# Kernel tuning notes

Hardware: AMD Instinct MI355X
Metric: run time of the kernel (lower is better)

## Reference

```python
import jax, jax.numpy as jnp
import numpy as np

N_HEAD, D_MODEL, D_K, D_V = 16, 1024, 64, 64
BN_EPS = 1e-5
NEG_INF = -1e9


def setup_inputs() -> dict:
    key = jax.random.key(0)
    ks = jax.random.split(key, 10)
    B, L = 4, 1024
    q = jax.random.normal(ks[0], (B, L, D_MODEL), dtype=jnp.float32)
    k = jax.random.normal(ks[1], (B, L, D_MODEL), dtype=jnp.float32)
    v = jax.random.normal(ks[2], (B, L, D_MODEL), dtype=jnp.float32)
    attn_mask = jax.random.randint(ks[3], (B, L, L), 0, 2) == 1  # True -> masked out
    s = 1.0 / np.sqrt(D_MODEL)
    w_qs = jax.random.normal(ks[4], (N_HEAD, D_MODEL, D_K), dtype=jnp.float32) * s
    w_ks = jax.random.normal(ks[5], (N_HEAD, D_MODEL, D_K), dtype=jnp.float32) * s
    w_vs = jax.random.normal(ks[6], (N_HEAD, D_MODEL, D_V), dtype=jnp.float32) * s
    proj_w = jax.random.normal(ks[7], (D_MODEL, N_HEAD * D_V), dtype=jnp.float32) * s
    proj_b = jnp.zeros((D_MODEL,), dtype=jnp.float32)
    bn_gamma = jnp.ones((D_MODEL,), dtype=jnp.float32)
    bn_beta = jnp.zeros((D_MODEL,), dtype=jnp.float32)
    return {"q": q, "k": k, "v": v, "attn_mask": attn_mask,
            "w_qs": w_qs, "w_ks": w_ks, "w_vs": w_vs,
            "proj_w": proj_w, "proj_b": proj_b,
            "bn_gamma": bn_gamma, "bn_beta": bn_beta}


def reference(q, k, v, attn_mask, w_qs, w_ks, w_vs, proj_w, proj_b, bn_gamma, bn_beta):
    B, Lq, D = q.shape
    temper = jnp.asarray(np.sqrt(D), dtype=q.dtype)
    residual = q
    # per-head projections: (H, B, L, dk)
    qh = jnp.einsum('bld,hdk->hblk', q, w_qs)
    kh = jnp.einsum('bld,hdk->hblk', k, w_ks)
    vh = jnp.einsum('bld,hdv->hblv', v, w_vs)
    # scaled dot-product attention, temper = sqrt(d_model)
    scores = jnp.einsum('hbqk,hbsk->hbqs', qh, kh) / temper
    scores = jnp.where(attn_mask[None], NEG_INF, scores)
    attns = jax.nn.softmax(scores, axis=-1)  # (H, B, Lq, Lk)
    out_h = jnp.einsum('hbqs,hbsv->hbqv', attns, vh)  # (H, B, Lq, dv)
    # concat heads along feature dim in head order
    out = jnp.transpose(out_h, (1, 2, 0, 3)).reshape(B, Lq, N_HEAD * D_V)
    out = out @ proj_w.T + proj_b
    # residual + BatchNorm1d over channel dim (batch stats, training-mode math)
    x = out + residual  # (B, L, D)
    mean = jnp.mean(x, axis=(0, 1))
    var = jnp.var(x, axis=(0, 1))
    x = (x - mean) * jax.lax.rsqrt(var + BN_EPS) * bn_gamma + bn_beta
    attns_flat = attns.reshape(N_HEAD * B, Lq, -1)
    return x, attns_flat
```

## Files before the change

kernel.cpp:

```cpp
#include <hip/hip_runtime.h>

typedef unsigned short ushort;
typedef __attribute__((ext_vector_type(4))) float floatx4;
typedef __bf16 bf16x8 __attribute__((ext_vector_type(8)));
typedef __bf16 bf16x4 __attribute__((ext_vector_type(4)));
typedef float f32x4 __attribute__((ext_vector_type(4)));

constexpr int NB = 4;
constexpr int NL = 1024;
constexpr int ND = 1024;
constexpr int NH = 16;
constexpr int NDK = 64;

union B4 { bf16x4 v; unsigned long long ll; };

__device__ __forceinline__ void st_bf(ushort* dst, float f){
  union { __bf16 h; ushort u; } z; z.h = (__bf16)f; *dst = z.u;
}

#define MFMA(a,b,c) __builtin_amdgcn_mfma_f32_16x16x32_bf16((a),(b),(c),0,0,0)

__global__ __launch_bounds__(256) void k_prep(const float* __restrict__ q,
                                              const float* __restrict__ k,
                                              const float* __restrict__ v,
                                              const float* __restrict__ pw,
                                              const float* __restrict__ w0,
                                              const float* __restrict__ w1,
                                              const float* __restrict__ w2,
                                              const int* __restrict__ M,
                                              ushort* __restrict__ qb,
                                              ushort* __restrict__ kb,
                                              ushort* __restrict__ vb,
                                              ushort* __restrict__ pwb,
                                              ushort* __restrict__ t0,
                                              ushort* __restrict__ t1,
                                              ushort* __restrict__ t2,
                                              unsigned long long* __restrict__ MB,
                                              float* __restrict__ part){
  __shared__ ushort T[64][65];
  const int bid = blockIdx.x;
  const int tid = threadIdx.x;

  if (bid < 6656){
    const int a = (bid < 2048) ? 0 : (bid < 4096) ? 1 : (bid < 6144) ? 2 : 3;
    const int rel = bid - a * 2048;
    const float* src = (a == 0) ? q : (a == 1) ? k : (a == 2) ? v : pw;
    ushort* dst = (a == 0) ? qb : (a == 1) ? kb : (a == 2) ? vb : pwb;
    const size_t base = ((size_t)rel * 256 + tid) * 8;
    floatx4 v0 = *(const floatx4*)(src + base);
    floatx4 v1 = *(const floatx4*)(src + base + 4);
    bf16x8 o;
    #pragma unroll
    for (int j = 0; j < 4; j++){ o[j] = (__bf16)v0[j]; o[4 + j] = (__bf16)v1[j]; }
    *(bf16x8*)(dst + base) = o;
    return;
  }
  if (bid < 7424){
    const int r = bid - 6656;
    const int z = r >> 8;
    const int h = (r >> 4) & 15, k0 = (r & 15) * 64;
    const float* src = (z == 0) ? w0 : (z == 1) ? w1 : w2;
    ushort* dst = (z == 0) ? t0 : (z == 1) ? t1 : t2;
    const int qd = tid >> 6, lo = tid & 63;
    #pragma unroll
    for (int i = 0; i < 16; i++){
      int kl = qd + i * 4;
      float f = src[((size_t)h * 1024 + k0 + kl) * 64 + lo];
      union { __bf16 h2; ushort u; } zz; zz.h2 = (__bf16)f;
      T[kl][lo] = zz.u;
    }
    __syncthreads();
    #pragma unroll
    for (int i = 0; i < 16; i++){
      int dk = qd + i * 4;
      dst[((size_t)h * 64 + dk) * 1024 + k0 + lo] = T[lo][dk];
    }
    return;
  }
  if (bid < 11520){
    const int r = bid - 7424;
    #pragma unroll
    for (int rep = 0; rep < 4; rep++){
      const int gid = r * 1024 + rep * 256 + tid;
      const int widx = gid >> 6;
      int m = M[(size_t)widx * 64 + (gid & 63)];
      unsigned long long bal = __ballot(m != 0);
      if ((gid & 63) == 0) MB[widx] = bal;
    }
    return;
  }
  *(floatx4*)(part + tid * 8) = f32x4{0.f, 0.f, 0.f, 0.f};
  *(floatx4*)(part + tid * 8 + 4) = f32x4{0.f, 0.f, 0.f, 0.f};
}

__global__ __launch_bounds__(256) void k_projm(const ushort* __restrict__ qbp,
                                               const ushort* __restrict__ kbp,
                                               const ushort* __restrict__ vbp,
                                               const ushort* __restrict__ wqT,
                                               const ushort* __restrict__ wkT,
                                               const ushort* __restrict__ wvT,
                                               ushort* __restrict__ qh,
                                               ushort* __restrict__ kh,
                                               ushort* __restrict__ vt){
  __shared__ bf16x8 Ach[8 * 128];
  __shared__ bf16x8 Bch[8 * 128];
  const int z = blockIdx.z;
  const ushort* Xb = (z == 0) ? qbp : (z == 1) ? kbp : vbp;
  const ushort* WT = (z == 0) ? wqT : (z == 1) ? wkT : wvT;
  const int tid = threadIdx.x;
  const int lane = tid & 63, wid = tid >> 6;
  const int g = lane >> 4, c = lane & 15;
  const int d = blockIdx.y * 8 + blockIdx.x;
  const int tile = (d & 7) * 32 + (d >> 3);
  const int row0 = (tile >> 3) * 128, col0 = (tile & 7) * 128;
  const int wm = (wid >> 1) * 64, wn = (wid & 1) * 64;

  f32x4 zero = {0.f, 0.f, 0.f, 0.f};
  f32x4 acc[4][4];
  #pragma unroll
  for (int i = 0; i < 4; i++)
    #pragma unroll
    for (int j = 0; j < 4; j++) acc[i][j] = zero;

  for (int k0 = 0; k0 < ND; k0 += 64){
    #pragma unroll
    for (int i = 0; i < 4; i++){
      int e = tid + i * 256;
      int kc = e & 7, m = e >> 3;
      Ach[kc * 128 + (m ^ kc)] = *(const bf16x8*)(Xb + (size_t)(row0 + m) * ND + k0 + kc * 8);
    }
    #pragma unroll
    for (int i = 0; i < 4; i++){
      int e = tid + i * 256;
      int kc = e & 7, n = e >> 3;
      int hh = (col0 + n) >> 6, dk = (col0 + n) & 63;
      Bch[kc * 128 + (n ^ kc)] = *(const bf16x8*)(WT + ((size_t)(hh << 6) + dk) * 1024 + k0 + kc * 8);
    }
    __syncthreads();
    bf16x8 bfr[4][2];
    #pragma unroll
    for (int ni = 0; ni < 4; ni++){
      int n = wn + ni * 16 + c;
      bfr[ni][0] = Bch[g * 128 + (n ^ g)];
      bfr[ni][1] = Bch[(4 + g) * 128 + (n ^ (4 + g))];
    }
    #pragma unroll
    for (int mi = 0; mi < 4; mi++){
      int m = wm + mi * 16 + c;
      bf16x8 a0 = Ach[g * 128 + (m ^ g)];
      bf16x8 a1 = Ach[(4 + g) * 128 + (m ^ (4 + g))];
      #pragma unroll
      for (int ni = 0; ni < 4; ni++){
        acc[mi][ni] = MFMA(a0, bfr[ni][0], acc[mi][ni]);
        acc[mi][ni] = MFMA(a1, bfr[ni][1], acc[mi][ni]);
      }
    }
    __syncthreads();
  }
  if (z == 2){
    #pragma unroll
    for (int mi = 0; mi < 4; mi++){
      #pragma unroll
      for (int ni = 0; ni < 4; ni++){
        int n = col0 + wn + ni * 16 + c;
        int hh = n >> 6, dk = n & 63;
        int m0 = row0 + wm + mi * 16 + g * 4;
        int bb = m0 >> 10, l = m0 & 1023;
        B4 o;
        #pragma unroll
        for (int r = 0; r < 4; r++) o.v[r] = (__bf16)acc[mi][ni][r];
        *(unsigned long long*)(vt + (((size_t)hh * NB + bb) * 64 + dk) * 1024 + l) = o.ll;
      }
    }
  } else {
    ushort* OUT = (z == 0) ? qh : kh;
    #pragma unroll
    for (int mi = 0; mi < 4; mi++){
      #pragma unroll
      for (int ni = 0; ni < 4; ni++){
        #pragma unroll
        for (int r = 0; r < 4; r++){
          int m = row0 + wm + mi * 16 + g * 4 + r;
          int n = col0 + wn + ni * 16 + c;
          int bb = m >> 10, ls = m & 1023;
          int hh = n >> 6, dk = n & 63;
          st_bf(OUT + (((size_t)hh * NB + bb) * NL + ls) * NDK + dk, acc[mi][ni][r]);
        }
      }
    }
  }
}

__global__ __launch_bounds__(256, 4) void k_attn(const ushort* __restrict__ QH,
                                                 const ushort* __restrict__ KH,
                                                 const ushort* __restrict__ VT,
                                                 const unsigned* __restrict__ MB,
                                                 float* __restrict__ ATT,
                                                 ushort* __restrict__ CTX){
  __shared__ bf16x8 Kch[512];
  __shared__ bf16x8 Vch[512];
  __shared__ ushort Ps[4][16][72];
  __shared__ unsigned Ms[64 * 33];
  const int tid = threadIdx.x;
  const int lane = tid & 63, wid = tid >> 6;
  const int g = lane >> 4, c = lane & 15;
  const int d = blockIdx.y * 16 + blockIdx.x;
  const int tile = (d & 7) * 128 + (d >> 3);
  const int hb = tile >> 4;
  const int q0 = (tile & 15) * 64;
  const int h = hb >> 2, b = hb & 3;

  const int q = q0 + wid * 16 + c;
  const size_t qkbase = (size_t)hb * NL;

  bf16x8 qf0 = *(const bf16x8*)(QH + (qkbase + q) * NDK + g * 8);
  bf16x8 qf1 = *(const bf16x8*)(QH + (qkbase + q) * NDK + 32 + g * 8);

  {
    const unsigned* mbase = MB + ((size_t)(b << 10) + q0) * 32;
    #pragma unroll
    for (int i = 0; i < 8; i++){
      int idx = tid + i * 256;
      int ql2 = idx >> 5, word = idx & 31;
      Ms[ql2 * 33 + word] = mbase[ql2 * 32 + word];
    }
  }
  const int ql = wid * 16 + c;
  const int mg = g * 4;

  float rs = 0.f;
  for (int t = 0; t < 16; ++t){
    __syncthreads();
    const ushort* ksrc = KH + (qkbase + t * 64) * NDK;
    #pragma unroll
    for (int i = 0; i < 2; i++){
      int idx = tid * 2 + i;
      int sr = idx >> 3, kc = idx & 7;
      Kch[sr * 8 + (kc ^ (sr & 7))] = *(const bf16x8*)(ksrc + idx * 8);
    }
    __syncthreads();
    #pragma unroll
    for (int sub2 = 0; sub2 < 4; ++sub2){
      int s = sub2 * 16 + c;
      bf16x8 kf0 = Kch[s * 8 + (g ^ (s & 7))];
      bf16x8 kf1 = Kch[s * 8 + ((4 + g) ^ (s & 7))];
      f32x4 a = {0.f, 0.f, 0.f, 0.f};
      a = MFMA(kf0, qf0, a);
      a = MFMA(kf1, qf1, a);
      unsigned w = Ms[ql * 33 + t * 2 + (sub2 >> 1)];
      unsigned bits4 = (w >> (((sub2 & 1) << 4) + mg)) & 0xFu;
      #pragma unroll
      for (int r = 0; r < 4; r++)
        rs += ((bits4 >> r) & 1u) ? 0.f : __expf(a[r] * (1.f / 32.f));
    }
  }
  rs += __shfl_xor(rs, 16);
  rs += __shfl_xor(rs, 32);
  const float invd = 1.f / rs;

  f32x4 zero = {0.f, 0.f, 0.f, 0.f};
  f32x4 acc[4];
  #pragma unroll
  for (int i = 0; i < 4; i++) acc[i] = zero;

  for (int t = 0; t < 16; ++t){
    __syncthreads();
    const ushort* ksrc = KH + (qkbase + t * 64) * NDK;
    #pragma unroll
    for (int i = 0; i < 2; i++){
      int idx = tid * 2 + i;
      int sr = idx >> 3, kc = idx & 7;
      Kch[sr * 8 + (kc ^ (sr & 7))] = *(const bf16x8*)(ksrc + idx * 8);
    }
    #pragma unroll
    for (int i = 0; i < 2; i++){
      int idx = tid + i * 256;
      int dv = idx >> 3, kc = idx & 7;
      Vch[kc * 64 + (dv ^ kc)] = *(const bf16x8*)(VT + ((size_t)hb * 64 + dv) * 1024 + t * 64 + kc * 8);
    }
    __syncthreads();
    #pragma unroll
    for (int sub2 = 0; sub2 < 4; ++sub2){
      int s = sub2 * 16 + c;
      bf16x8 kf0 = Kch[s * 8 + (g ^ (s & 7))];
      bf16x8 kf1 = Kch[s * 8 + ((4 + g) ^ (s & 7))];
      f32x4 a = {0.f, 0.f, 0.f, 0.f};
      a = MFMA(kf0, qf0, a);
      a = MFMA(kf1, qf1, a);
      unsigned w = Ms[ql * 33 + t * 2 + (sub2 >> 1)];
      unsigned bits4 = (w >> (((sub2 & 1) << 4) + mg)) & 0xFu;
      floatx4 pn;
      B4 pw;
      #pragma unroll
      for (int r = 0; r < 4; r++){
        float p = ((bits4 >> r) & 1u) ? 0.f : __expf(a[r] * (1.f / 32.f)) * invd;
        pn[r] = p;
        pw.v[r] = (__bf16)p;
      }
      __builtin_nontemporal_store(pn,
        (floatx4*)(ATT + ((size_t)hb * NL + q) * NL + (t * 4 + sub2) * 16 + g * 4));
      *(unsigned long long*)&Ps[wid][c][sub2 * 16 + g * 4] = pw.ll;
    }
    #pragma unroll
    for (int ss = 0; ss < 2; ++ss){
      bf16x8 afr = *(bf16x8*)&Ps[wid][c][ss * 32 + g * 8];
      #pragma unroll
      for (int ni = 0; ni < 4; ni++){
        int kcr = ss * 4 + g;
        bf16x8 vfr = Vch[kcr * 64 + ((ni * 16 + c) ^ kcr)];
        acc[ni] = MFMA(afr, vfr, acc[ni]);
      }
    }
  }

  #pragma unroll
  for (int ni = 0; ni < 4; ni++)
    #pragma unroll
    for (int r = 0; r < 4; r++){
      int qq = q0 + wid * 16 + g * 4 + r;
      int dv = ni * 16 + c;
      st_bf(CTX + ((size_t)b * NL + qq) * ND + h * NDK + dv, acc[ni][r]);
    }
}

__global__ __launch_bounds__(256) void k_projo(const ushort* __restrict__ CTX,
                                               const ushort* __restrict__ PWb,
                                               const float* __restrict__ PB,
                                               const float* __restrict__ RES,
                                               float* __restrict__ X,
                                               float* __restrict__ part){
  __shared__ bf16x8 Ach[8 * 128];
  __shared__ bf16x8 Bch[8 * 128];
  const int tid = threadIdx.x;
  const int lane = tid & 63, wid = tid >> 6;
  const int g = lane >> 4, c = lane & 15;
  const int d = blockIdx.y * 8 + blockIdx.x;
  const int tile = (d & 7) * 32 + (d >> 3);
  const int row0 = (tile >> 3) * 128, col0 = (tile & 7) * 128;
  const int wm = (wid >> 1) * 64, wn = (wid & 1) * 64;

  f32x4 zero = {0.f, 0.f, 0.f, 0.f};
  f32x4 acc[4][4];
  #pragma unroll
  for (int i = 0; i < 4; i++)
    #pragma unroll
    for (int j = 0; j < 4; j++) acc[i][j] = zero;

  for (int k0 = 0; k0 < ND; k0 += 64){
    #pragma unroll
    for (int i = 0; i < 4; i++){
      int e = tid + i * 256;
      int kc = e & 7, m = e >> 3;
      Ach[kc * 128 + (m ^ kc)] = *(const bf16x8*)(CTX + (size_t)(row0 + m) * ND + k0 + kc * 8);
    }
    #pragma unroll
    for (int i = 0; i < 4; i++){
      int e = tid + i * 256;
      int kc = e & 7, n = e >> 3;
      Bch[kc * 128 + (n ^ kc)] = *(const bf16x8*)(PWb + (size_t)(col0 + n) * 1024 + k0 + kc * 8);
    }
    __syncthreads();
    bf16x8 bfr[4][2];
    #pragma unroll
    for (int ni = 0; ni < 4; ni++){
      int n = wn + ni * 16 + c;
      bfr[ni][0] = Bch[g * 128 + (n ^ g)];
      bfr[ni][1] = Bch[(4 + g) * 128 + (n ^ (4 + g))];
    }
    #pragma unroll
    for (int mi = 0; mi < 4; mi++){
      int m = wm + mi * 16 + c;
      bf16x8 a0 = Ach[g * 128 + (m ^ g)];
      bf16x8 a1 = Ach[(4 + g) * 128 + (m ^ (4 + g))];
      #pragma unroll
      for (int ni = 0; ni < 4; ni++){
        acc[mi][ni] = MFMA(a0, bfr[ni][0], acc[mi][ni]);
        acc[mi][ni] = MFMA(a1, bfr[ni][1], acc[mi][ni]);
      }
    }
    __syncthreads();
  }
  float s_[4] = {0.f, 0.f, 0.f, 0.f}, s2_[4] = {0.f, 0.f, 0.f, 0.f};
  #pragma unroll
  for (int mi = 0; mi < 4; mi++)
    #pragma unroll
    for (int ni = 0; ni < 4; ni++)
      #pragma unroll
      for (int r = 0; r < 4; r++){
        int m = row0 + wm + mi * 16 + g * 4 + r;
        int n = col0 + wn + ni * 16 + c;
        float rv = __builtin_nontemporal_load(RES + (size_t)m * ND + n);
        float val = acc[mi][ni][r] + PB[n] + rv;
        X[(size_t)m * ND + n] = val;
        s_[ni] += val; s2_[ni] += val * val;
      }
  #pragma unroll
  for (int ni = 0; ni < 4; ni++){
    float a = s_[ni], b2 = s2_[ni];
    a += __shfl_xor(a, 16); b2 += __shfl_xor(b2, 16);
    a += __shfl_xor(a, 32); b2 += __shfl_xor(b2, 32);
    if (g == 0){
      int n = col0 + wn + ni * 16 + c;
      atomicAdd(&part[n], a);
      atomicAdd(&part[1024 + n], b2);
    }
  }
}

__global__ __launch_bounds__(256) void k_bnapply(float* __restrict__ X,
                                                 const float* __restrict__ part,
                                                 const float* __restrict__ G,
                                                 const float* __restrict__ Bt){
  const int idx = blockIdx.x * 256 + threadIdx.x;
  const size_t base = (size_t)idx * 8;
  const int d0 = (int)(base & (ND - 1));
  floatx4 x0 = *(const floatx4*)(X + base);
  floatx4 x1 = *(const floatx4*)(X + base + 4);
  floatx4 o0, o1;
  constexpr float invN = 1.f / (NB * NL);
  #pragma unroll
  for (int e = 0; e < 4; e++){
    int d = d0 + e;
    float mean = part[d] * invN;
    float var = part[1024 + d] * invN - mean * mean;
    float rstd = rsqrtf(var + 1e-5f);
    o0[e] = (x0[e] - mean) * rstd * G[d] + Bt[d];
    int d2 = d0 + 4 + e;
    float mean2 = part[d2] * invN;
    float var2 = part[1024 + d2] * invN - mean2 * mean2;
    float rstd2 = rsqrtf(var2 + 1e-5f);
    o1[e] = (x1[e] - mean2) * rstd2 * G[d2] + Bt[d2];
  }
  __builtin_nontemporal_store(o0, (floatx4*)(X + base));
  __builtin_nontemporal_store(o1, (floatx4*)(X + base + 4));
}

extern "C" void kernel_launch(void* const* d_in, const int* in_sizes, int n_in,
                              void* d_out, int out_size, void* d_ws, size_t ws_size,
                              hipStream_t stream){
  const float* q      = (const float*)d_in[0];
  const float* k      = (const float*)d_in[1];
  const float* v      = (const float*)d_in[2];
  const int*   mask   = (const int*)d_in[3];
  const float* w_qs   = (const float*)d_in[4];
  const float* w_ks   = (const float*)d_in[5];
  const float* w_vs   = (const float*)d_in[6];
  const float* proj_w = (const float*)d_in[7];
  const float* proj_b = (const float*)d_in[8];
  const float* gamma  = (const float*)d_in[9];
  const float* beta   = (const float*)d_in[10];

  float* out_x   = (float*)d_out;
  float* out_att = out_x + (size_t)NB * NL * ND;

  char* ws = (char*)d_ws;
  ushort* qb  = (ushort*)(ws);
  ushort* kb  = (ushort*)(ws + (8u  << 20));
  ushort* vb  = (ushort*)(ws + (16u << 20));
  ushort* qh  = (ushort*)(ws + (24u << 20));
  ushort* kh  = (ushort*)(ws + (32u << 20));
  ushort* vt  = (ushort*)(ws + (40u << 20));
  ushort* wqT = (ushort*)(ws + (48u << 20));
  ushort* wkT = (ushort*)(ws + (50u << 20));
  ushort* wvT = (ushort*)(ws + (52u << 20));
  ushort* pwb = (ushort*)(ws + (54u << 20));
  unsigned long long* mb = (unsigned long long*)(ws + (56u << 20));
  float*  part = (float*)(ws + (57u << 20));
  ushort* ctx  = qb;

  dim3 blk(256);
  k_prep<<<dim3(11521), blk, 0, stream>>>(q, k, v, proj_w, w_qs, w_ks, w_vs, mask,
                                          qb, kb, vb, pwb, wqT, wkT, wvT, mb, part);
  k_projm<<<dim3(8, 32, 3), blk, 0, stream>>>(qb, kb, vb, wqT, wkT, wvT, qh, kh, vt);
  k_attn<<<dim3(16, 64), blk, 0, stream>>>(qh, kh, vt, (const unsigned*)mb, out_att, ctx);
  k_projo<<<dim3(8, 32), blk, 0, stream>>>(ctx, pwb, proj_b, q, out_x, part);
  k_bnapply<<<dim3(NB * NL * ND / 8 / 256), blk, 0, stream>>>(out_x, part, gamma, beta);
}
```

Before: 205.3 us.

## Double-buffer K/V tiles in attention, fold softmax scale into exp2

The attention kernel moves to 512-thread blocks covering 128 queries and double-buffers the K and V tiles in shared memory. Each tile's global loads are prefetched into registers during compute, so one barrier per iteration replaces two. The softmax scale and log2(e) are folded into Q at projection time, and the 1/sum normaliser enters as a log2 bias in the MFMA accumulator, so each probability needs only a single exp2. Nontemporal loads and stores are replaced with ordinary ones, and the larger blocks change occupancy and the tile ordering.

```diff
diff --git a/kernel.cpp b/kernel.cpp
--- a/kernel.cpp
+++ b/kernel.cpp
@@ -11,6 +11,8 @@
 constexpr int ND = 1024;
 constexpr int NH = 16;
 constexpr int NDK = 64;
+
+#define QSCALE 0.045084230079650879f
 
 union B4 { bf16x4 v; unsigned long long ll; };
 
@@ -174,6 +176,7 @@
     }
   } else {
     ushort* OUT = (z == 0) ? qh : kh;
+    const float sc = (z == 0) ? QSCALE : 1.0f;
     #pragma unroll
     for (int mi = 0; mi < 4; mi++){
       #pragma unroll
@@ -184,30 +187,29 @@
           int n = col0 + wn + ni * 16 + c;
           int bb = m >> 10, ls = m & 1023;
           int hh = n >> 6, dk = n & 63;
-          st_bf(OUT + (((size_t)hh * NB + bb) * NL + ls) * NDK + dk, acc[mi][ni][r]);
+          st_bf(OUT + (((size_t)hh * NB + bb) * NL + ls) * NDK + dk, acc[mi][ni][r] * sc);
         }
       }
     }
   }
 }
 
-__global__ __launch_bounds__(256, 4) void k_attn(const ushort* __restrict__ QH,
+__global__ __launch_bounds__(512, 4) void k_attn(const ushort* __restrict__ QH,
                                                  const ushort* __restrict__ KH,
                                                  const ushort* __restrict__ VT,
                                                  const unsigned* __restrict__ MB,
                                                  float* __restrict__ ATT,
                                                  ushort* __restrict__ CTX){
-  __shared__ bf16x8 Kch[512];
-  __shared__ bf16x8 Vch[512];
-  __shared__ ushort Ps[4][16][72];
-  __shared__ unsigned Ms[64 * 33];
+  __shared__ bf16x8 Kch[2][512];
+  __shared__ bf16x8 Vch[2][512];
+  __shared__ ushort Ps[8][16][72];
+  __shared__ unsigned Ms[128 * 33];
   const int tid = threadIdx.x;
   const int lane = tid & 63, wid = tid >> 6;
   const int g = lane >> 4, c = lane & 15;
-  const int d = blockIdx.y * 16 + blockIdx.x;
-  const int tile = (d & 7) * 128 + (d >> 3);
-  const int hb = tile >> 4;
-  const int q0 = (tile & 15) * 64;
+  const int tile = blockIdx.x * 64 + blockIdx.y;
+  const int hb = tile >> 3;
+  const int q0 = (tile & 7) * 128;
   const int h = hb >> 2, b = hb & 3;
 
   const int q = q0 + wid * 16 + c;
@@ -220,7 +222,7 @@
     const unsigned* mbase = MB + ((size_t)(b << 10) + q0) * 32;
     #pragma unroll
     for (int i = 0; i < 8; i++){
-      int idx = tid + i * 256;
+      int idx = tid + i * 512;
       int ql2 = idx >> 5, word = idx & 31;
       Ms[ql2 * 33 + word] = mbase[ql2 * 32 + word];
     }
@@ -228,22 +230,22 @@
   const int ql = wid * 16 + c;
   const int mg = g * 4;
 
+  const int sr = tid >> 3, kc = tid & 7;
+  const int swzK = sr * 8 + (kc ^ (sr & 7));
+  const int swzV = kc * 64 + (sr ^ kc);
+
   float rs = 0.f;
+  bf16x8 kr = *(const bf16x8*)(KH + qkbase * NDK + tid * 8);
+  Kch[0][swzK] = kr;
   for (int t = 0; t < 16; ++t){
     __syncthreads();
-    const ushort* ksrc = KH + (qkbase + t * 64) * NDK;
-    #pragma unroll
-    for (int i = 0; i < 2; i++){
-      int idx = tid * 2 + i;
-      int sr = idx >> 3, kc = idx & 7;
-      Kch[sr * 8 + (kc ^ (sr & 7))] = *(const bf16x8*)(ksrc + idx * 8);
-    }
-    __syncthreads();
+    if (t < 15) kr = *(const bf16x8*)(KH + (qkbase + (t + 1) * 64) * NDK + tid * 8);
+    const bf16x8* Kc = Kch[t & 1];
     #pragma unroll
     for (int sub2 = 0; sub2 < 4; ++sub2){
       int s = sub2 * 16 + c;
-      bf16x8 kf0 = Kch[s * 8 + (g ^ (s & 7))];
-      bf16x8 kf1 = Kch[s * 8 + ((4 + g) ^ (s & 7))];
+      bf16x8 kf0 = Kc[s * 8 + (g ^ (s & 7))];
+      bf16x8 kf1 = Kc[s * 8 + ((4 + g) ^ (s & 7))];
       f32x4 a = {0.f, 0.f, 0.f, 0.f};
       a = MFMA(kf0, qf0, a);
       a = MFMA(kf1, qf1, a);
@@ -251,40 +253,39 @@
       unsigned bits4 = (w >> (((sub2 & 1) << 4) + mg)) & 0xFu;
       #pragma unroll
       for (int r = 0; r < 4; r++)
-        rs += ((bits4 >> r) & 1u) ? 0.f : __expf(a[r] * (1.f / 32.f));
-    }
+        rs += ((bits4 >> r) & 1u) ? 0.f : __builtin_amdgcn_exp2f(a[r]);
+    }
+    if (t < 15) Kch[(t + 1) & 1][swzK] = kr;
   }
   rs += __shfl_xor(rs, 16);
   rs += __shfl_xor(rs, 32);
   const float invd = 1.f / rs;
-
-  f32x4 zero = {0.f, 0.f, 0.f, 0.f};
+  const float lsh = -__log2f(rs);
+
   f32x4 acc[4];
   #pragma unroll
-  for (int i = 0; i < 4; i++) acc[i] = zero;
+  for (int i = 0; i < 4; i++) acc[i] = f32x4{0.f, 0.f, 0.f, 0.f};
+  const f32x4 cin = {lsh, lsh, lsh, lsh};
+
+  kr = *(const bf16x8*)(KH + qkbase * NDK + tid * 8);
+  bf16x8 vr = *(const bf16x8*)(VT + ((size_t)hb * 64 + sr) * 1024 + kc * 8);
+  Kch[0][swzK] = kr;
+  Vch[0][swzV] = vr;
 
   for (int t = 0; t < 16; ++t){
     __syncthreads();
-    const ushort* ksrc = KH + (qkbase + t * 64) * NDK;
-    #pragma unroll
-    for (int i = 0; i < 2; i++){
-      int idx = tid * 2 + i;
-      int sr = idx >> 3, kc = idx & 7;
-      Kch[sr * 8 + (kc ^ (sr & 7))] = *(const bf16x8*)(ksrc + idx * 8);
-    }
-    #pragma unroll
-    for (int i = 0; i < 2; i++){
-      int idx = tid + i * 256;
-      int dv = idx >> 3, kc = idx & 7;
-      Vch[kc * 64 + (dv ^ kc)] = *(const bf16x8*)(VT + ((size_t)hb * 64 + dv) * 1024 + t * 64 + kc * 8);
-    }
-    __syncthreads();
+    if (t < 15){
+      kr = *(const bf16x8*)(KH + (qkbase + (t + 1) * 64) * NDK + tid * 8);
+      vr = *(const bf16x8*)(VT + ((size_t)hb * 64 + sr) * 1024 + (t + 1) * 64 + kc * 8);
+    }
+    const bf16x8* Kc = Kch[t & 1];
+    const bf16x8* Vc = Vch[t & 1];
     #pragma unroll
     for (int sub2 = 0; sub2 < 4; ++sub2){
       int s = sub2 * 16 + c;
-      bf16x8 kf0 = Kch[s * 8 + (g ^ (s & 7))];
-      bf16x8 kf1 = Kch[s * 8 + ((4 + g) ^ (s & 7))];
-      f32x4 a = {0.f, 0.f, 0.f, 0.f};
+      bf16x8 kf0 = Kc[s * 8 + (g ^ (s & 7))];
+      bf16x8 kf1 = Kc[s * 8 + ((4 + g) ^ (s & 7))];
+      f32x4 a = cin;
       a = MFMA(kf0, qf0, a);
       a = MFMA(kf1, qf1, a);
       unsigned w = Ms[ql * 33 + t * 2 + (sub2 >> 1)];
@@ -293,12 +294,11 @@
       B4 pw;
       #pragma unroll
       for (int r = 0; r < 4; r++){
-        float p = ((bits4 >> r) & 1u) ? 0.f : __expf(a[r] * (1.f / 32.f)) * invd;
+        float p = ((bits4 >> r) & 1u) ? 0.f : __builtin_amdgcn_exp2f(a[r]);
         pn[r] = p;
         pw.v[r] = (__bf16)p;
       }
-      __builtin_nontemporal_store(pn,
-        (floatx4*)(ATT + ((size_t)hb * NL + q) * NL + (t * 4 + sub2) * 16 + g * 4));
+      *(floatx4*)(ATT + ((size_t)hb * NL + q) * NL + (t * 4 + sub2) * 16 + g * 4) = pn;
       *(unsigned long long*)&Ps[wid][c][sub2 * 16 + g * 4] = pw.ll;
     }
     #pragma unroll
@@ -307,9 +307,13 @@
       #pragma unroll
       for (int ni = 0; ni < 4; ni++){
         int kcr = ss * 4 + g;
-        bf16x8 vfr = Vch[kcr * 64 + ((ni * 16 + c) ^ kcr)];
+        bf16x8 vfr = Vc[kcr * 64 + ((ni * 16 + c) ^ kcr)];
         acc[ni] = MFMA(afr, vfr, acc[ni]);
       }
+    }
+    if (t < 15){
+      Kch[(t + 1) & 1][swzK] = kr;
+      Vch[(t + 1) & 1][swzV] = vr;
     }
   }
 
@@ -389,8 +393,7 @@
       for (int r = 0; r < 4; r++){
         int m = row0 + wm + mi * 16 + g * 4 + r;
         int n = col0 + wn + ni * 16 + c;
-        float rv = __builtin_nontemporal_load(RES + (size_t)m * ND + n);
-        float val = acc[mi][ni][r] + PB[n] + rv;
+        float val = acc[mi][ni][r] + PB[n] + RES[(size_t)m * ND + n];
         X[(size_t)m * ND + n] = val;
         s_[ni] += val; s2_[ni] += val * val;
       }
@@ -431,8 +434,8 @@
     float rstd2 = rsqrtf(var2 + 1e-5f);
     o1[e] = (x1[e] - mean2) * rstd2 * G[d2] + Bt[d2];
   }
-  __builtin_nontemporal_store(o0, (floatx4*)(X + base));
-  __builtin_nontemporal_store(o1, (floatx4*)(X + base + 4));
+  *(floatx4*)(X + base) = o0;
+  *(floatx4*)(X + base + 4) = o1;
 }
 
 extern "C" void kernel_launch(void* const* d_in, const int* in_sizes, int n_in,
@@ -472,7 +475,7 @@
   k_prep<<<dim3(11521), blk, 0, stream>>>(q, k, v, proj_w, w_qs, w_ks, w_vs, mask,
                                           qb, kb, vb, pwb, wqT, wkT, wvT, mb, part);
   k_projm<<<dim3(8, 32, 3), blk, 0, stream>>>(qb, kb, vb, wqT, wkT, wvT, qh, kh, vt);
-  k_attn<<<dim3(16, 64), blk, 0, stream>>>(qh, kh, vt, (const unsigned*)mb, out_att, ctx);
+  k_attn<<<dim3(8, 64), dim3(512), 0, stream>>>(qh, kh, vt, (const unsigned*)mb, out_att, ctx);
   k_projo<<<dim3(8, 32), blk, 0, stream>>>(ctx, pwb, proj_b, q, out_x, part);
   k_bnapply<<<dim3(NB * NL * ND / 8 / 256), blk, 0, stream>>>(out_x, part, gamma, beta);
 }
```

Result: faster. 191.2 us (-6.9%).
